# Kernel optimization log

Hardware: AMD Instinct MI355X
Metric: run time of the kernel (lower is better)

Reference implementation:

```python
import jax, jax.numpy as jnp
import numpy as np

L = 3        # layer_num
D = 64       # hidden_size (input_dim)
NU = 100000  # user nodes in batched graph
NI = 100000  # item nodes in batched graph
NUSER = 200000  # user vocab
NITEM = 200000  # item vocab
E = 1000000  # edges per relation ('by' and 'pby')
B = 1024     # target users per batch


def _time_enc(t, freq, phase):
    # TimeEncode: cos(t * basis_freq + phase), per edge -> [E, D]
    return jnp.cos(t[:, None] * freq[None, :] + phase[None, :])


def _seg_attn(e, vals, dst, num_seg):
    # softmax of e over edges sharing a destination node, then weighted sum of vals
    m = jax.ops.segment_max(e, dst, num_segments=num_seg)
    ex = jnp.exp(e - m[dst])
    denom = jax.ops.segment_sum(ex, dst, num_segments=num_seg)
    alpha = ex / denom[dst]
    return jax.ops.segment_sum(alpha[:, None] * vals, dst, num_segments=num_seg)


def _forward(user_emb, item_emb, Wu, Wi, Wuu, Wii,
             u_freq, u_phase, uk_freq, uk_phase,
             i_freq, i_phase, ik_freq, ik_phase,
             unified_W, dense_W, dense_b,
             by_time, pby_time,
             user_id, item_id, by_src, by_dst, pby_src, pby_dst,
             user_index, last_item_index):
    nu = user_id.shape[0]
    ni = item_id.shape[0]
    d = user_emb.shape[1]
    scale = 1.0 / jnp.sqrt(jnp.float32(d))
    user_h = user_emb[user_id]   # [NU, D]
    item_h = item_emb[item_id]   # [NI, D]
    user_layers = []
    n_layers = Wu.shape[0]
    for l in range(n_layers):
        uh = user_h @ Wu[l]   # user_weight
        ih = item_h @ Wi[l]   # item_weight
        # --- 'by' relation: item -> user (user_reduce_func) ---
        src_i = ih[by_src]    # mailbox['item_h']
        dst_u = uh[by_dst]    # mailbox['user_h'] (dst feature)
        e_u = jnp.sum((_time_enc(by_time, u_freq[l], u_phase[l]) + src_i) * dst_u, -1) * scale
        agg_u = _seg_attn(e_u, src_i + _time_enc(by_time, uk_freq[l], uk_phase[l]), by_dst, nu)
        # --- 'pby' relation: user -> item (item_reduce_func) ---
        src_u = uh[pby_src]
        dst_i = ih[pby_dst]
        e_i = jnp.sum((_time_enc(pby_time, i_freq[l], i_phase[l]) + src_u) * dst_i, -1) * scale
        agg_i = _seg_attn(e_i, src_u + _time_enc(pby_time, ik_freq[l], ik_phase[l]), pby_dst, ni)
        # node update: elu(W [agg ; old])
        user_h = jax.nn.elu(jnp.concatenate([agg_u, user_h], -1) @ Wuu[l])
        item_h = jax.nn.elu(jnp.concatenate([agg_i, item_h], -1) @ Wii[l])
        user_layers.append(user_h[user_index])
    user_layers.append(item_h[last_item_index])  # last_item=True
    unified = jnp.concatenate(user_layers, -1) @ unified_W
    return jax.nn.relu(unified @ dense_W + dense_b)  # [B, 3]


def setup_inputs() -> dict:
    key = jax.random.key(0)
    ks = jax.random.split(key, 20)
    w = lambda k, shape: jax.random.normal(k, shape, jnp.float32) * 0.05
    freq0 = jnp.asarray(1.0 / 10 ** np.linspace(0, 9, D), dtype=jnp.float32)
    freq = jnp.tile(freq0[None], (L, 1))
    zph = jnp.zeros((L, D), jnp.float32)
    return {
        'user_emb': w(ks[0], (NUSER, D)),
        'item_emb': w(ks[1], (NITEM, D)),
        'Wu': w(ks[2], (L, D, D)),
        'Wi': w(ks[3], (L, D, D)),
        'Wuu': w(ks[4], (L, 2 * D, D)),
        'Wii': w(ks[5], (L, 2 * D, D)),
        'u_freq': freq, 'u_phase': zph,
        'uk_freq': freq, 'uk_phase': zph,
        'i_freq': freq, 'i_phase': zph,
        'ik_freq': freq, 'ik_phase': zph,
        'unified_W': w(ks[6], ((L + 1) * D, D)),
        'dense_W': w(ks[7], (D, 3)),
        'dense_b': jnp.zeros((3,), jnp.float32),
        'by_time': jax.random.uniform(ks[8], (E,), jnp.float32),
        'pby_time': jax.random.uniform(ks[9], (E,), jnp.float32),
        'user_id': jax.random.randint(ks[10], (NU,), 0, NUSER),
        'item_id': jax.random.randint(ks[11], (NI,), 0, NITEM),
        'by_src': jax.random.randint(ks[12], (E,), 0, NI),
        'by_dst': jax.random.randint(ks[13], (E,), 0, NU),
        'pby_src': jax.random.randint(ks[14], (E,), 0, NU),
        'pby_dst': jax.random.randint(ks[15], (E,), 0, NI),
        'user_index': jax.random.randint(ks[16], (B,), 0, NU),
        'last_item_index': jax.random.randint(ks[17], (B,), 0, NI),
    }


def reference(user_emb, item_emb, Wu, Wi, Wuu, Wii,
              u_freq, u_phase, uk_freq, uk_phase,
              i_freq, i_phase, ik_freq, ik_phase,
              unified_W, dense_W, dense_b,
              by_time, pby_time,
              user_id, item_id, by_src, by_dst, pby_src, pby_dst,
              user_index, last_item_index):
    return _forward(user_emb, item_emb, Wu, Wi, Wuu, Wii,
                    u_freq, u_phase, uk_freq, uk_phase,
                    i_freq, i_phase, ik_freq, ik_phase,
                    unified_W, dense_W, dense_b,
                    by_time, pby_time,
                    user_id, item_id, by_src, by_dst, pby_src, pby_dst,
                    user_index, last_item_index)
```

## Files before the change

### kernel.cpp

```cpp
#include <hip/hip_runtime.h>
#include <math.h>

#define D 64
#define NB 1024
#define CHUNKE 4096

typedef __attribute__((ext_vector_type(8))) short s8bf;
typedef __attribute__((ext_vector_type(4))) float fx4;
typedef __attribute__((ext_vector_type(4))) int ix4;

__device__ __forceinline__ float bf2f(unsigned short u) {
    union { unsigned int i; float f; } v; v.i = ((unsigned int)u) << 16; return v.f;
}
__device__ __forceinline__ unsigned short f2bf(float f) {
    union { float f; unsigned int i; } v; v.f = f;
    unsigned int r = v.i + 0x7FFFu + ((v.i >> 16) & 1u);
    return (unsigned short)(r >> 16);
}

__global__ __launch_bounds__(256) void k_gather2(const float* __restrict__ ue,
                                                 const float* __restrict__ ie,
                                                 const int* __restrict__ uid,
                                                 const int* __restrict__ iid,
                                                 unsigned short* __restrict__ uh0,
                                                 unsigned short* __restrict__ ih0, int NU, int NI) {
    int i = blockIdx.x * blockDim.x + threadIdx.x;
    if (i >= (NU + NI) * D) return;
    int r = i >> 6, c = i & 63;
    if (r < NU) uh0[(size_t)r * D + c] = f2bf(ue[(size_t)uid[r] * D + c]);
    else { int j = r - NU; ih0[(size_t)j * D + c] = f2bf(ie[(size_t)iid[j] * D + c]); }
}

__global__ __launch_bounds__(256) void k_wprep(const float* __restrict__ Wu,
                                               const float* __restrict__ Wi,
                                               const float* __restrict__ Wuu,
                                               const float* __restrict__ Wii,
                                               unsigned short* __restrict__ WuT,
                                               unsigned short* __restrict__ WiT,
                                               unsigned short* __restrict__ WuuT,
                                               unsigned short* __restrict__ WiiT, int L) {
    int i = blockIdx.x * blockDim.x + threadIdx.x;
    int n1 = L * 64 * 64, n2 = L * 64 * 128;
    if (i < n1) {
        int l = i >> 12, c = (i >> 6) & 63, k = i & 63;
        WuT[i] = f2bf(Wu[l * 4096 + k * 64 + c]);
        WiT[i] = f2bf(Wi[l * 4096 + k * 64 + c]);
    }
    if (i < n2) {
        int l = i >> 13, c = (i >> 7) & 63, k = i & 127;
        WuuT[i] = f2bf(Wuu[l * 8192 + k * 64 + c]);
        WiiT[i] = f2bf(Wii[l * 8192 + k * 64 + c]);
    }
}

__global__ __launch_bounds__(256) void k_hist2(const int* __restrict__ bd,
                                               const int* __restrict__ pd,
                                               int* __restrict__ cu, int* __restrict__ ci, int E) {
    for (int i = blockIdx.x * blockDim.x + threadIdx.x; i < 2 * E; i += gridDim.x * blockDim.x) {
        if (i < E) atomicAdd(&cu[bd[i]], 1);
        else       atomicAdd(&ci[pd[i - E]], 1);
    }
}

__global__ __launch_bounds__(256) void k_scan_block2(const int* __restrict__ cu, int* __restrict__ rp_u,
                                                     const int* __restrict__ ci, int* __restrict__ rp_i,
                                                     int* __restrict__ bsums, int nbU, int NU, int NI) {
    __shared__ int ts[256];
    bool rel = blockIdx.x >= (unsigned)nbU;
    const int* in = rel ? ci : cu;
    int* out = rel ? rp_i : rp_u;
    int n = rel ? NI : NU;
    int boff = rel ? blockIdx.x - nbU : blockIdx.x;
    int t = threadIdx.x;
    int base = boff * 2048 + t * 8;
    int v[8]; int s = 0;
#pragma unroll
    for (int k = 0; k < 8; ++k) { int idx = base + k; v[k] = idx < n ? in[idx] : 0; s += v[k]; }
    ts[t] = s; __syncthreads();
    for (int off = 1; off < 256; off <<= 1) {
        int x = (t >= off) ? ts[t - off] : 0;
        __syncthreads(); ts[t] += x; __syncthreads();
    }
    int excl = ts[t] - s;
    if (t == 255) bsums[blockIdx.x] = ts[255];
    int run = excl;
#pragma unroll
    for (int k = 0; k < 8; ++k) { int idx = base + k; if (idx < n) out[idx] = run; run += v[k]; }
}

__global__ __launch_bounds__(256) void k_scan_small(int* __restrict__ bsums, int nbU, int nbI) {
    __shared__ int ts[256];
    int t = threadIdx.x;
    int half = t >> 7, local = t & 127;
    int nb = half ? nbI : nbU;
    int g = half ? nbU + local : local;
    int v = local < nb ? bsums[g] : 0;
    ts[t] = v; __syncthreads();
    for (int off = 1; off < 128; off <<= 1) {
        int x = (local >= off) ? ts[t - off] : 0;
        __syncthreads(); ts[t] += x; __syncthreads();
    }
    if (local < nb) bsums[g] = ts[t] - v;
}

__global__ __launch_bounds__(256) void k_fixup2(int* __restrict__ rp_u, int* __restrict__ rp_i,
                                                const int* __restrict__ bsums,
                                                int* __restrict__ cu, int* __restrict__ ci,
                                                int NU, int NI, int E, int nbU) {
    int i = blockIdx.x * blockDim.x + threadIdx.x;
    if (i < NU) {
        int v = rp_u[i] + bsums[i >> 11]; rp_u[i] = v; cu[i] = v;
        if (i == 0) rp_u[NU] = E;
    } else if (i < NU + NI) {
        int j = i - NU;
        int v = rp_i[j] + bsums[nbU + (j >> 11)]; rp_i[j] = v; ci[j] = v;
        if (j == 0) rp_i[NI] = E;
    }
}

__global__ __launch_bounds__(256) void k_phist(const int* __restrict__ bd,
                                               const int* __restrict__ pd,
                                               int* __restrict__ H, int E, int nwgE,
                                               unsigned npbU, unsigned npbI) {
    bool rel = blockIdx.x >= (unsigned)nwgE;
    int wg = rel ? blockIdx.x - nwgE : blockIdx.x;
    const int* dsts = rel ? pd : bd;
    unsigned npb = rel ? npbI : npbU;
    int* Hr = H + (rel ? NB * nwgE : 0);
    __shared__ int hist[NB];
    int t = threadIdx.x;
    for (int j = t; j < NB; j += 256) hist[j] = 0;
    __syncthreads();
    int base = wg * CHUNKE;
#pragma unroll
    for (int k = 0; k < CHUNKE / 256; ++k) {
        int e = base + t + k * 256;
        if (e < E) atomicAdd(&hist[(unsigned)dsts[e] / npb], 1);
    }
    __syncthreads();
    for (int j = t; j < NB; j += 256) Hr[j * nwgE + wg] = hist[j];
}

__global__ __launch_bounds__(256) void k_gscan_block(const int* __restrict__ in,
                                                     int* __restrict__ out,
                                                     int* __restrict__ bsums, int n) {
    __shared__ int ts[256];
    int t = threadIdx.x;
    int base = blockIdx.x * 2048 + t * 8;
    int v[8]; int s = 0;
#pragma unroll
    for (int k = 0; k < 8; ++k) { int idx = base + k; v[k] = idx < n ? in[idx] : 0; s += v[k]; }
    ts[t] = s; __syncthreads();
    for (int off = 1; off < 256; off <<= 1) {
        int x = (t >= off) ? ts[t - off] : 0;
        __syncthreads(); ts[t] += x; __syncthreads();
    }
    int excl = ts[t] - s;
    if (t == 255) bsums[blockIdx.x] = ts[255];
    int run = excl;
#pragma unroll
    for (int k = 0; k < 8; ++k) { int idx = base + k; if (idx < n) out[idx] = run; run += v[k]; }
}

__global__ __launch_bounds__(256) void k_gscan_small(int* __restrict__ bsums, int nb) {
    __shared__ int ts[256];
    int t = threadIdx.x;
    int v = t < nb ? bsums[t] : 0;
    ts[t] = v; __syncthreads();
    for (int off = 1; off < 256; off <<= 1) {
        int x = (t >= off) ? ts[t - off] : 0;
        __syncthreads(); ts[t] += x; __syncthreads();
    }
    if (t < nb) bsums[t] = ts[t] - v;
}

__global__ __launch_bounds__(256) void k_gscan_fix(int* __restrict__ out,
                                                   const int* __restrict__ bsums, int n) {
    int i = blockIdx.x * blockDim.x + threadIdx.x;
    if (i < n) out[i] += bsums[i >> 11];
}

__global__ __launch_bounds__(256) void k_ppart(
    const int* __restrict__ bs, const int* __restrict__ bd, const float* __restrict__ bt,
    const int* __restrict__ ps, const int* __restrict__ pd, const float* __restrict__ pt,
    const int* __restrict__ H, ix4* __restrict__ stg_by, ix4* __restrict__ stg_pby,
    int E, int nwgE, unsigned npbU, unsigned npbI) {
    bool rel = blockIdx.x >= (unsigned)nwgE;
    int wg = rel ? blockIdx.x - nwgE : blockIdx.x;
    const int* srcs = rel ? ps : bs;
    const int* dsts = rel ? pd : bd;
    const float* tms = rel ? pt : bt;
    unsigned npb = rel ? npbI : npbU;
    const int* Hr = H + (rel ? NB * nwgE : 0);
    ix4* stg = rel ? stg_pby : stg_by;
    int sub = rel ? E : 0;
    __shared__ int cur[NB];
    int t = threadIdx.x;
    for (int j = t; j < NB; j += 256) cur[j] = Hr[j * nwgE + wg] - sub;
    __syncthreads();
    int base = wg * CHUNKE;
#pragma unroll
    for (int k = 0; k < CHUNKE / 256; ++k) {
        int e = base + t + k * 256;
        if (e < E) {
            int d = dsts[e];
            int pos = atomicAdd(&cur[(unsigned)d / npb], 1);
            ix4 v = {srcs[e], __float_as_int(tms[e]), d, 0};
            stg[pos] = v;
        }
    }
}

__global__ __launch_bounds__(256) void k_sortfin(
    const ix4* __restrict__ stg_by, const ix4* __restrict__ stg_pby,
    const int* __restrict__ rp_u, const int* __restrict__ rp_i,
    int* __restrict__ cu, int* __restrict__ ci,
    ix4* __restrict__ by_e, ix4* __restrict__ pby_e,
    int NU, int NI, int npbU, int npbI) {
    bool rel = blockIdx.x >= (unsigned)NB;
    int b = rel ? blockIdx.x - NB : blockIdx.x;
    const ix4* stg = rel ? stg_pby : stg_by;
    const int* rp = rel ? rp_i : rp_u;
    int* cur = rel ? ci : cu;
    ix4* out = rel ? pby_e : by_e;
    int n = rel ? NI : NU;
    int npb = rel ? npbI : npbU;
    long long s0 = (long long)b * npb; if (s0 > n) s0 = n;
    long long s1 = (long long)(b + 1) * npb; if (s1 > n) s1 = n;
    int beg = rp[s0], end = rp[s1];
    for (int j = beg + threadIdx.x; j < end; j += 256) {
        ix4 q = stg[j];
        int pos = atomicAdd(&cur[q.z], 1);
        out[pos] = q;
    }
}

__global__ __launch_bounds__(256) void k_transform4(
    const unsigned short* __restrict__ user_h, const unsigned short* __restrict__ item_h,
    const unsigned short* __restrict__ WuT_l, const unsigned short* __restrict__ WiT_l,
    unsigned short* __restrict__ uh, unsigned short* __restrict__ ih,
    int NU, int NI, int G) {
    bool rel = blockIdx.x >= (unsigned)G;
    int b = rel ? blockIdx.x - G : blockIdx.x;
    const unsigned short* in = rel ? item_h : user_h;
    const unsigned short* WT = rel ? WiT_l : WuT_l;
    unsigned short* out = rel ? ih : uh;
    int n = rel ? NI : NU;
    int lane = threadIdx.x & 63;
    int l15 = lane & 15, l4 = lane >> 4;
    s8bf bfr[8];
#pragma unroll
    for (int ct = 0; ct < 4; ++ct)
#pragma unroll
        for (int kk = 0; kk < 2; ++kk)
            bfr[ct * 2 + kk] = *(const s8bf*)&WT[(ct * 16 + l15) * 64 + kk * 32 + l4 * 8];
    int wave = b * 4 + (threadIdx.x >> 6);
    int nw = G * 4;
    int ntiles = (n + 15) >> 4;
    for (int t = wave; t < ntiles; t += nw) {
        int r = t * 16 + l15; if (r >= n) r = n - 1;
        s8bf afr0 = *(const s8bf*)&in[(size_t)r * 64 + l4 * 8];
        s8bf afr1 = *(const s8bf*)&in[(size_t)r * 64 + 32 + l4 * 8];
#pragma unroll
        for (int ct = 0; ct < 4; ++ct) {
            fx4 c = {0.f, 0.f, 0.f, 0.f};
            c = __builtin_amdgcn_mfma_f32_16x16x32_bf16(afr0, bfr[ct * 2 + 0], c, 0, 0, 0);
            c = __builtin_amdgcn_mfma_f32_16x16x32_bf16(afr1, bfr[ct * 2 + 1], c, 0, 0, 0);
#pragma unroll
            for (int i2 = 0; i2 < 4; ++i2) {
                int row = t * 16 + l4 * 4 + i2;
                if (row < n) out[(size_t)row * 64 + ct * 16 + l15] = f2bf(c[i2]);
            }
        }
    }
}

__global__ __launch_bounds__(256) void k_edge2(
    const unsigned short* __restrict__ ihF, const unsigned short* __restrict__ uhF,
    const ix4* __restrict__ by_e, const ix4* __restrict__ pby_e,
    const float* __restrict__ uf, const float* __restrict__ up,
    const float* __restrict__ ukf, const float* __restrict__ ukp,
    const float* __restrict__ ifq, const float* __restrict__ ipq,
    const float* __restrict__ ikf, const float* __restrict__ ikp,
    float* __restrict__ agg_u, float* __restrict__ den_u,
    float* __restrict__ agg_i, float* __restrict__ den_i,
    int E, int EB) {
    bool rel = blockIdx.x >= (unsigned)EB;
    int rblk = rel ? blockIdx.x - EB : blockIdx.x;
    const unsigned short* srcF = rel ? uhF : ihF;
    const unsigned short* dstF = rel ? ihF : uhF;
    const ix4* ee = rel ? pby_e : by_e;
    const float* efq = rel ? ifq : uf;
    const float* eps = rel ? ipq : up;
    const float* kfq = rel ? ikf : ukf;
    const float* kps = rel ? ikp : ukp;
    float* agg = rel ? agg_i : agg_u;
    float* den = rel ? den_i : den_u;

    int lane = threadIdx.x & 15;
    int grp  = threadIdx.x >> 4;
    int base = rblk * 256 + grp * 16;
    if (base >= E) return;
    float ef0 = efq[lane], ef1 = efq[lane + 16], ef2 = efq[lane + 32], ef3 = efq[lane + 48];
    float ep0 = eps[lane], ep1 = eps[lane + 16], ep2 = eps[lane + 32], ep3 = eps[lane + 48];
    float kf0 = kfq[lane], kf1 = kfq[lane + 16], kf2 = kfq[lane + 32], kf3 = kfq[lane + 48];
    float kp0 = kps[lane], kp1 = kps[lane + 16], kp2 = kps[lane + 32], kp3 = kps[lane + 48];
    bool same = ef0 == kf0 && ef1 == kf1 && ef2 == kf2 && ef3 == kf3 &&
                ep0 == kp0 && ep1 == kp1 && ep2 == kp2 && ep3 == kp3;
    same = __all(same);

    float a0 = 0, a1 = 0, a2 = 0, a3 = 0, dn = 0;
    float d0 = 0, d1 = 0, d2 = 0, d3 = 0;
    int cur = -1;
    for (int j = 0; j < 16; ++j) {
        int e = base + j;
        if (e >= E) break;
        ix4 q = ee[e];
        int s = q.x; float t = __int_as_float(q.y); int dd = q.z;
        if (dd != cur) {
            if (cur >= 0) {
                float* ap = &agg[(size_t)cur * D + lane];
                unsafeAtomicAdd(ap +  0, a0); unsafeAtomicAdd(ap + 16, a1);
                unsafeAtomicAdd(ap + 32, a2); unsafeAtomicAdd(ap + 48, a3);
                if (lane == 0) unsafeAtomicAdd(&den[cur], dn);
            }
            a0 = a1 = a2 = a3 = 0; dn = 0; cur = dd;
            const unsigned short* dp = &dstF[(size_t)dd * D + lane];
            d0 = bf2f(dp[0]); d1 = bf2f(dp[16]); d2 = bf2f(dp[32]); d3 = bf2f(dp[48]);
        }
        const unsigned short* sp = &srcF[(size_t)s * D + lane];
        float s0 = bf2f(sp[0]), s1 = bf2f(sp[16]), s2 = bf2f(sp[32]), s3 = bf2f(sp[48]);
        float c0 = __cosf(fmaf(t, ef0, ep0));
        float c1 = __cosf(fmaf(t, ef1, ep1));
        float c2 = __cosf(fmaf(t, ef2, ep2));
        float c3 = __cosf(fmaf(t, ef3, ep3));
        float p = (c0 + s0) * d0 + (c1 + s1) * d1 + (c2 + s2) * d2 + (c3 + s3) * d3;
        p += __shfl_xor(p, 1); p += __shfl_xor(p, 2);
        p += __shfl_xor(p, 4); p += __shfl_xor(p, 8);
        float ex = __expf(p * 0.125f);
        float k0, k1, k2, k3;
        if (same) { k0 = c0; k1 = c1; k2 = c2; k3 = c3; }
        else {
            k0 = __cosf(fmaf(t, kf0, kp0)); k1 = __cosf(fmaf(t, kf1, kp1));
            k2 = __cosf(fmaf(t, kf2, kp2)); k3 = __cosf(fmaf(t, kf3, kp3));
        }
        a0 = fmaf(ex, s0 + k0, a0); a1 = fmaf(ex, s1 + k1, a1);
        a2 = fmaf(ex, s2 + k2, a2); a3 = fmaf(ex, s3 + k3, a3);
        dn += ex;
    }
    if (cur >= 0) {
        float* ap = &agg[(size_t)cur * D + lane];
        unsafeAtomicAdd(ap +  0, a0); unsafeAtomicAdd(ap + 16, a1);
        unsafeAtomicAdd(ap + 32, a2); unsafeAtomicAdd(ap + 48, a3);
        if (lane == 0) unsafeAtomicAdd(&den[cur], dn);
    }
}

__global__ __launch_bounds__(256) void k_update4(
    unsigned short* __restrict__ user_h, unsigned short* __restrict__ item_h,
    const float* __restrict__ agg_u, const float* __restrict__ den_u,
    const float* __restrict__ agg_i, const float* __restrict__ den_i,
    const unsigned short* __restrict__ WuuT_l, const unsigned short* __restrict__ WiiT_l,
    int NU, int NI, int G) {
    bool rel = blockIdx.x >= (unsigned)G;
    int b = rel ? blockIdx.x - G : blockIdx.x;
    unsigned short* h = rel ? item_h : user_h;
    const float* agg = rel ? agg_i : agg_u;
    const float* den = rel ? den_i : den_u;
    const unsigned short* WT = rel ? WiiT_l : WuuT_l;
    int n = rel ? NI : NU;
    int lane = threadIdx.x & 63;
    int l15 = lane & 15, l4 = lane >> 4;
    s8bf bfr[16];
#pragma unroll
    for (int ct = 0; ct < 4; ++ct)
#pragma unroll
        for (int kk = 0; kk < 4; ++kk)
            bfr[ct * 4 + kk] = *(const s8bf*)&WT[(ct * 16 + l15) * 128 + kk * 32 + l4 * 8];
    int wave = b * 4 + (threadIdx.x >> 6);
    int nw = G * 4;
    int ntiles = (n + 15) >> 4;
    for (int t = wave; t < ntiles; t += nw) {
        int r = t * 16 + l15; if (r >= n) r = n - 1;
        float dd = den[r];
        float inv = dd > 0.f ? 1.f / dd : 0.f;
        s8bf afr[4];
#pragma unroll
        for (int kk = 0; kk < 2; ++kk) {
            const float4* ap = (const float4*)&agg[(size_t)r * 64 + kk * 32 + l4 * 8];
            float4 x = ap[0], y = ap[1];
            s8bf f;
            f[0] = (short)f2bf(x.x * inv); f[1] = (short)f2bf(x.y * inv);
            f[2] = (short)f2bf(x.z * inv); f[3] = (short)f2bf(x.w * inv);
            f[4] = (short)f2bf(y.x * inv); f[5] = (short)f2bf(y.y * inv);
            f[6] = (short)f2bf(y.z * inv); f[7] = (short)f2bf(y.w * inv);
            afr[kk] = f;
        }
        afr[2] = *(const s8bf*)&h[(size_t)r * 64 + l4 * 8];
        afr[3] = *(const s8bf*)&h[(size_t)r * 64 + 32 + l4 * 8];
#pragma unroll
        for (int ct = 0; ct < 4; ++ct) {
            fx4 c = {0.f, 0.f, 0.f, 0.f};
            c = __builtin_amdgcn_mfma_f32_16x16x32_bf16(afr[0], bfr[ct * 4 + 0], c, 0, 0, 0);
            c = __builtin_amdgcn_mfma_f32_16x16x32_bf16(afr[1], bfr[ct * 4 + 1], c, 0, 0, 0);
            c = __builtin_amdgcn_mfma_f32_16x16x32_bf16(afr[2], bfr[ct * 4 + 2], c, 0, 0, 0);
            c = __builtin_amdgcn_mfma_f32_16x16x32_bf16(afr[3], bfr[ct * 4 + 3], c, 0, 0, 0);
#pragma unroll
            for (int i2 = 0; i2 < 4; ++i2) {
                int row = t * 16 + l4 * 4 + i2;
                if (row < n) {
                    float o = c[i2];
                    h[(size_t)row * 64 + ct * 16 + l15] =
                        f2bf(o > 0.f ? o : __expf(o) - 1.f);
                }
            }
        }
    }
}

__global__ __launch_bounds__(256) void k_gather_feat(const unsigned short* __restrict__ h,
                                                     const int* __restrict__ idx,
                                                     float* __restrict__ feat, int B,
                                                     int colOff, int FW) {
    int i = blockIdx.x * blockDim.x + threadIdx.x;
    if (i >= B * D) return;
    int b = i >> 6, c = i & 63;
    feat[(size_t)b * FW + colOff + c] = bf2f(h[(size_t)idx[b] * D + c]);
}

__global__ __launch_bounds__(64) void k_final(const float* __restrict__ feat,
                                              const float* __restrict__ uW,
                                              const float* __restrict__ dW,
                                              const float* __restrict__ db,
                                              float* __restrict__ out, int B, int FW) {
    __shared__ float fr[512];
    __shared__ float un[D];
    int b = blockIdx.x;
    int c = threadIdx.x;
    for (int i = c; i < FW; i += 64) fr[i] = feat[(size_t)b * FW + i];
    __syncthreads();
    float acc = 0.f;
    for (int d = 0; d < FW; ++d) acc += fr[d] * uW[d * D + c];
    un[c] = acc;
    __syncthreads();
    if (c < 3) {
        float o = db[c];
#pragma unroll
        for (int d = 0; d < D; ++d) o += un[d] * dW[d * 3 + c];
        out[b * 3 + c] = o > 0.f ? o : 0.f;
    }
}

extern "C" void kernel_launch(void* const* d_in, const int* in_sizes, int n_in,
                              void* d_out, int out_size, void* d_ws, size_t ws_size,
                              hipStream_t stream) {
    const float* user_emb = (const float*)d_in[0];
    const float* item_emb = (const float*)d_in[1];
    const float* Wu       = (const float*)d_in[2];
    const float* Wi       = (const float*)d_in[3];
    const float* Wuu      = (const float*)d_in[4];
    const float* Wii      = (const float*)d_in[5];
    const float* u_freq   = (const float*)d_in[6];
    const float* u_phase  = (const float*)d_in[7];
    const float* uk_freq  = (const float*)d_in[8];
    const float* uk_phase = (const float*)d_in[9];
    const float* i_freq   = (const float*)d_in[10];
    const float* i_phase  = (const float*)d_in[11];
    const float* ik_freq  = (const float*)d_in[12];
    const float* ik_phase = (const float*)d_in[13];
    const float* unified_W = (const float*)d_in[14];
    const float* dense_W   = (const float*)d_in[15];
    const float* dense_b   = (const float*)d_in[16];
    const float* by_time   = (const float*)d_in[17];
    const float* pby_time  = (const float*)d_in[18];
    const int* user_id   = (const int*)d_in[19];
    const int* item_id   = (const int*)d_in[20];
    const int* by_src    = (const int*)d_in[21];
    const int* by_dst    = (const int*)d_in[22];
    const int* pby_src   = (const int*)d_in[23];
    const int* pby_dst   = (const int*)d_in[24];
    const int* user_index = (const int*)d_in[25];
    const int* last_item_index = (const int*)d_in[26];

    const int NU = in_sizes[19];
    const int NI = in_sizes[20];
    const int E  = in_sizes[21];
    const int B  = in_sizes[25];
    const int L  = in_sizes[2] / (D * D);
    const int FW = (L + 1) * D;
    const int npbU = (NU + NB - 1) / NB;
    const int npbI = (NI + NB - 1) / NB;
    const int nwgE = (E + CHUNKE - 1) / CHUNKE;

    char* wp = (char*)d_ws;
    auto alloc_f = [&](size_t n) { float* p = (float*)wp; wp += n * sizeof(float); return p; };
    auto alloc_i = [&](size_t n) { int* p = (int*)wp; wp += n * sizeof(int); return p; };
    auto alloc_i4 = [&](size_t n) { ix4* p = (ix4*)wp; wp += n * sizeof(ix4); return p; };
    auto alloc_h = [&](size_t n) { unsigned short* p = (unsigned short*)wp; wp += n * sizeof(unsigned short); return p; };
    float* agg_u = alloc_f((size_t)NU * D);
    float* agg_i = alloc_f((size_t)NI * D);
    float* den_u = alloc_f(NU);
    float* den_i = alloc_f(NI);
    size_t zero_bytes = (size_t)(wp - (char*)d_ws);
    ix4* by_e    = alloc_i4(E);
    ix4* pby_e   = alloc_i4(E);
    ix4* stg_by  = alloc_i4(E);
    ix4* stg_pby = alloc_i4(E);
    int* cur_u = alloc_i(NU);
    int* cur_i = alloc_i(NI);
    size_t cur_bytes = (size_t)NU * 4 + (size_t)NI * 4;
    unsigned short* user_h = alloc_h((size_t)NU * D);
    unsigned short* item_h = alloc_h((size_t)NI * D);
    unsigned short* uh = alloc_h((size_t)NU * D);
    unsigned short* ih = alloc_h((size_t)NI * D);
    unsigned short* WuT  = alloc_h((size_t)L * 64 * 64);
    unsigned short* WiT  = alloc_h((size_t)L * 64 * 64);
    unsigned short* WuuT = alloc_h((size_t)L * 64 * 128);
    unsigned short* WiiT = alloc_h((size_t)L * 64 * 128);
    int*   by_rowptr  = alloc_i(NU + 2);
    int*   pby_rowptr = alloc_i(NI + 2);
    int*   bsums      = alloc_i(512);
    int*   H          = alloc_i((size_t)2 * NB * nwgE);
    int*   gbsums     = alloc_i(512);
    float* feat       = alloc_f((size_t)B * FW);

    const int nbU = (NU + 2047) / 2048, nbI = (NI + 2047) / 2048;

    k_gather2<<<((NU + NI) * D + 255) / 256, 256, 0, stream>>>(
        user_emb, item_emb, user_id, item_id, user_h, item_h, NU, NI);
    k_wprep<<<(L * 64 * 128 + 255) / 256, 256, 0, stream>>>(Wu, Wi, Wuu, Wii,
                                                            WuT, WiT, WuuT, WiiT, L);

    hipMemsetAsync(cur_u, 0, cur_bytes, stream);
    k_hist2<<<2048, 256, 0, stream>>>(by_dst, pby_dst, cur_u, cur_i, E);
    k_scan_block2<<<nbU + nbI, 256, 0, stream>>>(cur_u, by_rowptr, cur_i, pby_rowptr,
                                                 bsums, nbU, NU, NI);
    k_scan_small<<<1, 256, 0, stream>>>(bsums, nbU, nbI);
    k_fixup2<<<(NU + NI + 255) / 256, 256, 0, stream>>>(by_rowptr, pby_rowptr, bsums,
                                                        cur_u, cur_i, NU, NI, E, nbU);

    k_phist<<<2 * nwgE, 256, 0, stream>>>(by_dst, pby_dst, H, E, nwgE,
                                          (unsigned)npbU, (unsigned)npbI);
    {
        int n2 = 2 * NB * nwgE;
        int gb = (n2 + 2047) / 2048;
        k_gscan_block<<<gb, 256, 0, stream>>>(H, H, gbsums, n2);
        k_gscan_small<<<1, 256, 0, stream>>>(gbsums, gb);
        k_gscan_fix<<<(n2 + 255) / 256, 256, 0, stream>>>(H, gbsums, n2);
    }
    k_ppart<<<2 * nwgE, 256, 0, stream>>>(by_src, by_dst, by_time,
                                          pby_src, pby_dst, pby_time,
                                          H, stg_by, stg_pby, E, nwgE,
                                          (unsigned)npbU, (unsigned)npbI);
    k_sortfin<<<2 * NB, 256, 0, stream>>>(stg_by, stg_pby, by_rowptr, pby_rowptr,
                                          cur_u, cur_i, by_e, pby_e,
                                          NU, NI, npbU, npbI);

    const int EB = (E + 255) / 256;
    const int GM = 512;
    for (int l = 0; l < L; ++l) {
        hipMemsetAsync(d_ws, 0, zero_bytes, stream);
        k_transform4<<<2 * GM, 256, 0, stream>>>(user_h, item_h,
                                                 WuT + (size_t)l * 4096, WiT + (size_t)l * 4096,
                                                 uh, ih, NU, NI, GM);
        k_edge2<<<2 * EB, 256, 0, stream>>>(
            ih, uh, by_e, pby_e,
            u_freq + l * D, u_phase + l * D, uk_freq + l * D, uk_phase + l * D,
            i_freq + l * D, i_phase + l * D, ik_freq + l * D, ik_phase + l * D,
            agg_u, den_u, agg_i, den_i, E, EB);
        k_update4<<<2 * GM, 256, 0, stream>>>(user_h, item_h,
                                              agg_u, den_u, agg_i, den_i,
                                              WuuT + (size_t)l * 8192, WiiT + (size_t)l * 8192,
                                              NU, NI, GM);
        k_gather_feat<<<(B * D + 255) / 256, 256, 0, stream>>>(user_h, user_index, feat, B,
                                                               l * D, FW);
    }
    k_gather_feat<<<(B * D + 255) / 256, 256, 0, stream>>>(item_h, last_item_index, feat, B,
                                                           L * D, FW);
    k_final<<<B, 64, 0, stream>>>(feat, unified_W, dense_W, dense_b, (float*)d_out, B, FW);
}
```

Measured before the change: 697.3 us.

## Store edge aggregates in bf16 via packed atomics and fuse node histogram into partition histogram

The per-node aggregation buffers move from fp32 to bf16 and are accumulated with packed bf16 global atomics, which halves atomic traffic and buffer size. Edge-feature gathers now use 32-bit loads of bf16 pairs. The separate per-node degree histogram kernel is folded into the bucket histogram kernel so dst indices are read only once. Summing into bf16 with atomics loses precision, which may push results past tolerance.

After: 617.2 us. -11.5%, faster.

```diff
diff --git a/kernel.cpp b/kernel.cpp
--- a/kernel.cpp
+++ b/kernel.cpp
@@ -16,6 +16,10 @@
     union { float f; unsigned int i; } v; v.f = f;
     unsigned int r = v.i + 0x7FFFu + ((v.i >> 16) & 1u);
     return (unsigned short)(r >> 16);
+}
+__device__ __forceinline__ void atomAddPkBf16(unsigned short* addr, float a, float b) {
+    unsigned int pk = ((unsigned int)f2bf(b) << 16) | (unsigned int)f2bf(a);
+    asm volatile("global_atomic_pk_add_bf16 %0, %1, off" :: "v"(addr), "v"(pk) : "memory");
 }
 
 __global__ __launch_bounds__(256) void k_gather2(const float* __restrict__ ue,
@@ -53,15 +57,6 @@
     }
 }
 
-__global__ __launch_bounds__(256) void k_hist2(const int* __restrict__ bd,
-                                               const int* __restrict__ pd,
-                                               int* __restrict__ cu, int* __restrict__ ci, int E) {
-    for (int i = blockIdx.x * blockDim.x + threadIdx.x; i < 2 * E; i += gridDim.x * blockDim.x) {
-        if (i < E) atomicAdd(&cu[bd[i]], 1);
-        else       atomicAdd(&ci[pd[i - E]], 1);
-    }
-}
-
 __global__ __launch_bounds__(256) void k_scan_block2(const int* __restrict__ cu, int* __restrict__ rp_u,
                                                      const int* __restrict__ ci, int* __restrict__ rp_i,
                                                      int* __restrict__ bsums, int nbU, int NU, int NI) {
@@ -120,13 +115,16 @@
 
 __global__ __launch_bounds__(256) void k_phist(const int* __restrict__ bd,
                                                const int* __restrict__ pd,
-                                               int* __restrict__ H, int E, int nwgE,
+                                               int* __restrict__ H,
+                                               int* __restrict__ cu, int* __restrict__ ci,
+                                               int E, int nwgE,
                                                unsigned npbU, unsigned npbI) {
     bool rel = blockIdx.x >= (unsigned)nwgE;
     int wg = rel ? blockIdx.x - nwgE : blockIdx.x;
     const int* dsts = rel ? pd : bd;
     unsigned npb = rel ? npbI : npbU;
     int* Hr = H + (rel ? NB * nwgE : 0);
+    int* nodecnt = rel ? ci : cu;
     __shared__ int hist[NB];
     int t = threadIdx.x;
     for (int j = t; j < NB; j += 256) hist[j] = 0;
@@ -135,7 +133,11 @@
 #pragma unroll
     for (int k = 0; k < CHUNKE / 256; ++k) {
         int e = base + t + k * 256;
-        if (e < E) atomicAdd(&hist[(unsigned)dsts[e] / npb], 1);
+        if (e < E) {
+            int d = dsts[e];
+            atomicAdd(&hist[(unsigned)d / npb], 1);
+            atomicAdd(&nodecnt[d], 1);
+        }
     }
     __syncthreads();
     for (int j = t; j < NB; j += 256) Hr[j * nwgE + wg] = hist[j];
@@ -282,8 +284,8 @@
     const float* __restrict__ ukf, const float* __restrict__ ukp,
     const float* __restrict__ ifq, const float* __restrict__ ipq,
     const float* __restrict__ ikf, const float* __restrict__ ikp,
-    float* __restrict__ agg_u, float* __restrict__ den_u,
-    float* __restrict__ agg_i, float* __restrict__ den_i,
+    unsigned short* __restrict__ agg_u, float* __restrict__ den_u,
+    unsigned short* __restrict__ agg_i, float* __restrict__ den_i,
     int E, int EB) {
     bool rel = blockIdx.x >= (unsigned)EB;
     int rblk = rel ? blockIdx.x - EB : blockIdx.x;
@@ -294,19 +296,23 @@
     const float* eps = rel ? ipq : up;
     const float* kfq = rel ? ikf : ukf;
     const float* kps = rel ? ikp : ukp;
-    float* agg = rel ? agg_i : agg_u;
+    unsigned short* agg = rel ? agg_i : agg_u;
     float* den = rel ? den_i : den_u;
 
     int lane = threadIdx.x & 15;
     int grp  = threadIdx.x >> 4;
     int base = rblk * 256 + grp * 16;
     if (base >= E) return;
-    float ef0 = efq[lane], ef1 = efq[lane + 16], ef2 = efq[lane + 32], ef3 = efq[lane + 48];
-    float ep0 = eps[lane], ep1 = eps[lane + 16], ep2 = eps[lane + 32], ep3 = eps[lane + 48];
-    float kf0 = kfq[lane], kf1 = kfq[lane + 16], kf2 = kfq[lane + 32], kf3 = kfq[lane + 48];
-    float kp0 = kps[lane], kp1 = kps[lane + 16], kp2 = kps[lane + 32], kp3 = kps[lane + 48];
-    bool same = ef0 == kf0 && ef1 == kf1 && ef2 == kf2 && ef3 == kf3 &&
-                ep0 == kp0 && ep1 == kp1 && ep2 == kp2 && ep3 == kp3;
+    float2 ef01 = ((const float2*)efq)[lane];
+    float2 ef23 = ((const float2*)efq)[lane + 16];
+    float2 ep01 = ((const float2*)eps)[lane];
+    float2 ep23 = ((const float2*)eps)[lane + 16];
+    float2 kf01 = ((const float2*)kfq)[lane];
+    float2 kf23 = ((const float2*)kfq)[lane + 16];
+    float2 kp01 = ((const float2*)kps)[lane];
+    float2 kp23 = ((const float2*)kps)[lane + 16];
+    bool same = ef01.x == kf01.x && ef01.y == kf01.y && ef23.x == kf23.x && ef23.y == kf23.y &&
+                ep01.x == kp01.x && ep01.y == kp01.y && ep23.x == kp23.x && ep23.y == kp23.y;
     same = __all(same);
 
     float a0 = 0, a1 = 0, a2 = 0, a3 = 0, dn = 0;
@@ -319,21 +325,25 @@
         int s = q.x; float t = __int_as_float(q.y); int dd = q.z;
         if (dd != cur) {
             if (cur >= 0) {
-                float* ap = &agg[(size_t)cur * D + lane];
-                unsafeAtomicAdd(ap +  0, a0); unsafeAtomicAdd(ap + 16, a1);
-                unsafeAtomicAdd(ap + 32, a2); unsafeAtomicAdd(ap + 48, a3);
+                unsigned short* ap = &agg[(size_t)cur * D + 2 * lane];
+                atomAddPkBf16(ap, a0, a1);
+                atomAddPkBf16(ap + 32, a2, a3);
                 if (lane == 0) unsafeAtomicAdd(&den[cur], dn);
             }
             a0 = a1 = a2 = a3 = 0; dn = 0; cur = dd;
-            const unsigned short* dp = &dstF[(size_t)dd * D + lane];
-            d0 = bf2f(dp[0]); d1 = bf2f(dp[16]); d2 = bf2f(dp[32]); d3 = bf2f(dp[48]);
-        }
-        const unsigned short* sp = &srcF[(size_t)s * D + lane];
-        float s0 = bf2f(sp[0]), s1 = bf2f(sp[16]), s2 = bf2f(sp[32]), s3 = bf2f(sp[48]);
-        float c0 = __cosf(fmaf(t, ef0, ep0));
-        float c1 = __cosf(fmaf(t, ef1, ep1));
-        float c2 = __cosf(fmaf(t, ef2, ep2));
-        float c3 = __cosf(fmaf(t, ef3, ep3));
+            unsigned int u0 = *(const unsigned int*)&dstF[(size_t)dd * D + 2 * lane];
+            unsigned int u1 = *(const unsigned int*)&dstF[(size_t)dd * D + 32 + 2 * lane];
+            d0 = bf2f((unsigned short)u0); d1 = bf2f((unsigned short)(u0 >> 16));
+            d2 = bf2f((unsigned short)u1); d3 = bf2f((unsigned short)(u1 >> 16));
+        }
+        unsigned int s01 = *(const unsigned int*)&srcF[(size_t)s * D + 2 * lane];
+        unsigned int s23 = *(const unsigned int*)&srcF[(size_t)s * D + 32 + 2 * lane];
+        float s0 = bf2f((unsigned short)s01), s1 = bf2f((unsigned short)(s01 >> 16));
+        float s2 = bf2f((unsigned short)s23), s3 = bf2f((unsigned short)(s23 >> 16));
+        float c0 = __cosf(fmaf(t, ef01.x, ep01.x));
+        float c1 = __cosf(fmaf(t, ef01.y, ep01.y));
+        float c2 = __cosf(fmaf(t, ef23.x, ep23.x));
+        float c3 = __cosf(fmaf(t, ef23.y, ep23.y));
         float p = (c0 + s0) * d0 + (c1 + s1) * d1 + (c2 + s2) * d2 + (c3 + s3) * d3;
         p += __shfl_xor(p, 1); p += __shfl_xor(p, 2);
         p += __shfl_xor(p, 4); p += __shfl_xor(p, 8);
@@ -341,31 +351,31 @@
         float k0, k1, k2, k3;
         if (same) { k0 = c0; k1 = c1; k2 = c2; k3 = c3; }
         else {
-            k0 = __cosf(fmaf(t, kf0, kp0)); k1 = __cosf(fmaf(t, kf1, kp1));
-            k2 = __cosf(fmaf(t, kf2, kp2)); k3 = __cosf(fmaf(t, kf3, kp3));
+            k0 = __cosf(fmaf(t, kf01.x, kp01.x)); k1 = __cosf(fmaf(t, kf01.y, kp01.y));
+            k2 = __cosf(fmaf(t, kf23.x, kp23.x)); k3 = __cosf(fmaf(t, kf23.y, kp23.y));
         }
         a0 = fmaf(ex, s0 + k0, a0); a1 = fmaf(ex, s1 + k1, a1);
         a2 = fmaf(ex, s2 + k2, a2); a3 = fmaf(ex, s3 + k3, a3);
         dn += ex;
     }
     if (cur >= 0) {
-        float* ap = &agg[(size_t)cur * D + lane];
-        unsafeAtomicAdd(ap +  0, a0); unsafeAtomicAdd(ap + 16, a1);
-        unsafeAtomicAdd(ap + 32, a2); unsafeAtomicAdd(ap + 48, a3);
+        unsigned short* ap = &agg[(size_t)cur * D + 2 * lane];
+        atomAddPkBf16(ap, a0, a1);
+        atomAddPkBf16(ap + 32, a2, a3);
         if (lane == 0) unsafeAtomicAdd(&den[cur], dn);
     }
 }
 
 __global__ __launch_bounds__(256) void k_update4(
     unsigned short* __restrict__ user_h, unsigned short* __restrict__ item_h,
-    const float* __restrict__ agg_u, const float* __restrict__ den_u,
-    const float* __restrict__ agg_i, const float* __restrict__ den_i,
+    const unsigned short* __restrict__ agg_u, const float* __restrict__ den_u,
+    const unsigned short* __restrict__ agg_i, const float* __restrict__ den_i,
     const unsigned short* __restrict__ WuuT_l, const unsigned short* __restrict__ WiiT_l,
     int NU, int NI, int G) {
     bool rel = blockIdx.x >= (unsigned)G;
     int b = rel ? blockIdx.x - G : blockIdx.x;
     unsigned short* h = rel ? item_h : user_h;
-    const float* agg = rel ? agg_i : agg_u;
+    const unsigned short* agg = rel ? agg_i : agg_u;
     const float* den = rel ? den_i : den_u;
     const unsigned short* WT = rel ? WiiT_l : WuuT_l;
     int n = rel ? NI : NU;
@@ -387,13 +397,11 @@
         s8bf afr[4];
 #pragma unroll
         for (int kk = 0; kk < 2; ++kk) {
-            const float4* ap = (const float4*)&agg[(size_t)r * 64 + kk * 32 + l4 * 8];
-            float4 x = ap[0], y = ap[1];
+            s8bf a = *(const s8bf*)&agg[(size_t)r * 64 + kk * 32 + l4 * 8];
             s8bf f;
-            f[0] = (short)f2bf(x.x * inv); f[1] = (short)f2bf(x.y * inv);
-            f[2] = (short)f2bf(x.z * inv); f[3] = (short)f2bf(x.w * inv);
-            f[4] = (short)f2bf(y.x * inv); f[5] = (short)f2bf(y.y * inv);
-            f[6] = (short)f2bf(y.z * inv); f[7] = (short)f2bf(y.w * inv);
+#pragma unroll
+            for (int jj = 0; jj < 8; ++jj)
+                f[jj] = (short)f2bf(bf2f((unsigned short)a[jj]) * inv);
             afr[kk] = f;
         }
         afr[2] = *(const s8bf*)&h[(size_t)r * 64 + l4 * 8];
@@ -497,8 +505,8 @@
     auto alloc_i = [&](size_t n) { int* p = (int*)wp; wp += n * sizeof(int); return p; };
     auto alloc_i4 = [&](size_t n) { ix4* p = (ix4*)wp; wp += n * sizeof(ix4); return p; };
     auto alloc_h = [&](size_t n) { unsigned short* p = (unsigned short*)wp; wp += n * sizeof(unsigned short); return p; };
-    float* agg_u = alloc_f((size_t)NU * D);
-    float* agg_i = alloc_f((size_t)NI * D);
+    unsigned short* agg_u = alloc_h((size_t)NU * D);
+    unsigned short* agg_i = alloc_h((size_t)NI * D);
     float* den_u = alloc_f(NU);
     float* den_i = alloc_f(NI);
     size_t zero_bytes = (size_t)(wp - (char*)d_ws);
@@ -532,15 +540,13 @@
                                                             WuT, WiT, WuuT, WiiT, L);
 
     hipMemsetAsync(cur_u, 0, cur_bytes, stream);
-    k_hist2<<<2048, 256, 0, stream>>>(by_dst, pby_dst, cur_u, cur_i, E);
+    k_phist<<<2 * nwgE, 256, 0, stream>>>(by_dst, pby_dst, H, cur_u, cur_i, E, nwgE,
+                                          (unsigned)npbU, (unsigned)npbI);
     k_scan_block2<<<nbU + nbI, 256, 0, stream>>>(cur_u, by_rowptr, cur_i, pby_rowptr,
                                                  bsums, nbU, NU, NI);
     k_scan_small<<<1, 256, 0, stream>>>(bsums, nbU, nbI);
     k_fixup2<<<(NU + NI + 255) / 256, 256, 0, stream>>>(by_rowptr, pby_rowptr, bsums,
                                                         cur_u, cur_i, NU, NI, E, nbU);
-
-    k_phist<<<2 * nwgE, 256, 0, stream>>>(by_dst, pby_dst, H, E, nwgE,
-                                          (unsigned)npbU, (unsigned)npbI);
     {
         int n2 = 2 * NB * nwgE;
         int gb = (n2 + 2047) / 2048;
```
